# Optimization experiments

Measured on AMD Instinct MI355X. Metric: run time of the kernel, lower is better.

## Reference

```python
import jax, jax.numpy as jnp
import numpy as np
from jax.scipy.ndimage import map_coordinates

H = 256          # detector height (pixels)
W = 256          # detector width (pixels)
PX = 1.6875      # pixel size (mm); W*PX = 432mm
PIERCE = 216.0   # piercing point offset (mm) -> centered detector
SAD = 742.5      # source-to-isocenter distance (mm)
DAD = 517.15     # detector-to-isocenter distance (mm)


def _rotmat(angles):
    # ZYX intrinsic Euler rotation from (alpha, beta, gamma)
    a, b, g = angles[0], angles[1], angles[2]
    ca, sa = jnp.cos(a), jnp.sin(a)
    cb, sb = jnp.cos(b), jnp.sin(b)
    cg, sg = jnp.cos(g), jnp.sin(g)
    Rz = jnp.array([[ca, -sa, 0.], [sa, ca, 0.], [0., 0., 1.]])
    Ry = jnp.array([[cb, 0., sb], [0., 1., 0.], [-sb, 0., cb]])
    Rx = jnp.array([[1., 0., 0.], [0., cg, -sg], [0., sg, cg]])
    return Rz @ Ry @ Rx


def setup_inputs() -> dict:
    key = jax.random.key(0)
    k1, k2 = jax.random.split(key)
    volume = jax.random.uniform(k1, (256, 256, 256), dtype=jnp.float32)  # CT attenuation
    batch = jax.random.normal(k2, (2, 6), dtype=jnp.float32) * 0.1       # [B, (rot3, trans3)]
    return {"volume": volume, "batch": batch, "n_samples": 256}


def reference(volume, batch, n_samples):
    B = batch.shape[0]
    center = jnp.asarray(volume.shape, dtype=volume.dtype) / 2.0  # volume center (mm, unit spacing)

    rots = batch[:, 0:3]
    trans = batch[:, 3:6]
    R = jax.vmap(_rotmat)(rots)                              # [B,3,3]
    iso = center[None, :] + trans                            # [B,3]

    z = jnp.array([0., 0., 1.], dtype=volume.dtype)
    source = iso + SAD * jnp.einsum('bij,j->bi', R, z)       # [B,3]
    det_c = iso - DAD * jnp.einsum('bij,j->bi', R, z)        # [B,3]
    u_ax = R[:, :, 0]                                        # detector u axis [B,3]
    v_ax = R[:, :, 1]                                        # detector v axis [B,3]

    us = (jnp.arange(W, dtype=volume.dtype) * PX - PIERCE)   # [W]
    vs = (jnp.arange(H, dtype=volume.dtype) * PX - PIERCE)   # [H]
    # target pixel positions on detector plane: [B,H,W,3]
    target = (det_c[:, None, None, :]
              + us[None, None, :, None] * u_ax[:, None, None, :]
              + vs[None, :, None, None] * v_ax[:, None, None, :])

    ray = target - source[:, None, None, :]                  # [B,H,W,3]
    length = jnp.linalg.norm(ray, axis=-1)                   # [B,H,W]

    t = jnp.linspace(0.0, 1.0, n_samples, dtype=volume.dtype)  # [S]
    # sample points along each ray: [B,S,H,W,3] (voxel coords, unit spacing)
    pts = source[:, None, None, None, :] + t[None, :, None, None, None] * ray[:, None, :, :, :]

    def sample_one(p):  # p: [S,H,W,3]
        return map_coordinates(volume, [p[..., 0], p[..., 1], p[..., 2]], order=1, mode='constant', cval=0.0)

    samples = jax.vmap(sample_one)(pts)                      # [B,S,H,W]
    img = samples.sum(axis=1) * (length / n_samples)         # line integral [B,H,W]

    img = img.reshape(B, -1)                                 # [B, H*W]
    mn = img.min(axis=1, keepdims=True)
    mx = img.max(axis=1, keepdims=True)
    img = (img - mn) / (mx - mn)
    img = 1.0 - img                                          # bone_dark=True
    return img.reshape(B, H, W)
```

## Files before the change

kernel.cpp:

```cpp
#include <hip/hip_runtime.h>
#include <hip/hip_fp16.h>


static __device__ __constant__ float kPX     = 1.6875f;
static __device__ __constant__ float kPIERCE = 216.0f;
static __device__ __constant__ float kSAD    = 742.5f;
static __device__ __constant__ float kDAD    = 517.15f;

#define VOL_BYTES   (256u * 256u * 256u * 4u)
#define PAIR_R      258u
#define PAIR_ELEMS  (256u * 256u * PAIR_R)
#define PAIR_BYTES  (PAIR_ELEMS * 4u)

typedef __fp16 half2_raw __attribute__((ext_vector_type(2)));

__global__ void drr_init_mm(unsigned* mm) {
    int i = threadIdx.x;
    if (i < 4) mm[i] = (i & 1) ? 0u : 0x7F800000u;
}

__global__ __launch_bounds__(256) void drr_pack(const float* __restrict__ vol,
                                                __half2* __restrict__ vhp,
                                                float* __restrict__ raw) {
    const int bid = blockIdx.x;
    if (threadIdx.x < 32)
        raw[(bid << 5) + threadIdx.x] = 0.0f;

    __shared__ float tile[65][65];
    const int y    = bid >> 4;
    const int t4   = bid & 15;
    const int x0   = (t4 & 3) << 6;
    const int z0   = (t4 >> 2) << 6;

    const int rr = threadIdx.x >> 4;
    const int cc = threadIdx.x & 15;
    #pragma unroll
    for (int base = 0; base < 80; base += 16) {
        const int r = base + rr;
        if (r < 65) {
            const int x = x0 - 1 + r;
            float4 f = make_float4(0.0f, 0.0f, 0.0f, 0.0f);
            if (x >= 0)
                f = *(const float4*)&vol[(x << 16) | (y << 8) | (z0 + (cc << 2))];
            tile[r][(cc << 2) + 0] = f.x;
            tile[r][(cc << 2) + 1] = f.y;
            tile[r][(cc << 2) + 2] = f.z;
            tile[r][(cc << 2) + 3] = f.w;
        }
    }
    __syncthreads();

    const int lane = threadIdx.x & 63;
    const int row4 = threadIdx.x >> 6;
    for (int r = row4; r < 64; r += 4) {
        const int z = z0 + r;
        const unsigned base = (unsigned)((z << 8) | y) * PAIR_R;
        vhp[base + x0 + lane] =
            __halves2half2(__float2half(tile[lane][r]), __float2half(tile[lane + 1][r]));
    }
    if ((t4 & 3) == 3) {
        for (int r = row4; r < 64; r += 4) {
            const int z = z0 + r;
            const unsigned base = (unsigned)((z << 8) | y) * PAIR_R;
            if (lane == 0) {
                vhp[base + 256] = __halves2half2(__float2half(tile[64][r]), __float2half(0.0f));
                vhp[base + 257] = __halves2half2(__float2half(0.0f), __float2half(0.0f));
            }
        }
    }
}

__device__ __forceinline__ void slab(float s, float r, float lo, float hi,
                                     float& tlo, float& thi) {
    if (fabsf(r) > 1e-8f) {
        const float inv = 1.0f / r;
        const float ta  = (lo - s) * inv;
        const float tb  = (hi - s) * inv;
        tlo = fmaxf(tlo, fminf(ta, tb));
        thi = fminf(thi, fmaxf(ta, tb));
    } else if (s < lo || s > hi) {
        tlo = 2.0f; thi = -1.0f;
    }
}

struct RayCfg {
    float rx, ry, rz, length;
    int k_lo, k_hi;
    int s_lo, s_hi;
};

__device__ __forceinline__ void cfg_windows(float sx, float sy, float sz, RayCfg& c) {
    float tlo = 0.0f, thi = 1.0f;
    slab(sx, c.rx, -1.02f, 256.02f, tlo, thi);
    slab(sy, c.ry, -1.02f, 256.02f, tlo, thi);
    slab(sz, c.rz, -1.02f, 256.02f, tlo, thi);
    c.k_lo = 0; c.k_hi = -1;
    if (thi >= tlo) {
        c.k_lo = max(0,   (int)ceilf(tlo * 255.0f - 1e-3f));
        c.k_hi = min(255, (int)floorf(thi * 255.0f + 1e-3f));
    }
    float slo = 0.0f, shi = 1.0f;
    slab(sx, c.rx, 0.01f, 254.99f, slo, shi);
    slab(sy, c.ry, 0.01f, 254.99f, slo, shi);
    slab(sz, c.rz, 0.01f, 254.99f, slo, shi);
    c.s_lo = 1; c.s_hi = -1;
    if (shi >= slo) {
        c.s_lo = (int)ceilf(slo * 255.0f + 1e-3f);
        c.s_hi = (int)floorf(shi * 255.0f - 1e-3f);
    }
}

__device__ __forceinline__ void ray_setup2(const float* __restrict__ batch,
                                           int b, int u, int v0,
                                           float& sx, float& sy, float& sz,
                                           RayCfg& A, RayCfg& B) {
    const float a  = batch[b * 6 + 0];
    const float be = batch[b * 6 + 1];
    const float g  = batch[b * 6 + 2];
    const float tx = batch[b * 6 + 3];
    const float ty = batch[b * 6 + 4];
    const float tz = batch[b * 6 + 5];

    float sa, ca, sb, cb, sg, cg;
    sincosf(a, &sa, &ca);
    sincosf(be, &sb, &cb);
    sincosf(g, &sg, &cg);

    const float R00 = ca * cb;
    const float R01 = ca * sb * sg - sa * cg;
    const float R02 = sa * sg + ca * sb * cg;
    const float R10 = sa * cb;
    const float R11 = ca * cg + sa * sb * sg;
    const float R12 = sa * sb * cg - ca * sg;
    const float R20 = -sb;
    const float R21 = cb * sg;
    const float R22 = cb * cg;

    sx = 128.0f + tx + kSAD * R02;
    sy = 128.0f + ty + kSAD * R12;
    sz = 128.0f + tz + kSAD * R22;

    const float uu = u * kPX - kPIERCE;
    const float vv = v0 * kPX - kPIERCE;
    A.rx = uu * R00 + vv * R01 - (kSAD + kDAD) * R02;
    A.ry = uu * R10 + vv * R11 - (kSAD + kDAD) * R12;
    A.rz = uu * R20 + vv * R21 - (kSAD + kDAD) * R22;
    B.rx = A.rx + kPX * R01;
    B.ry = A.ry + kPX * R11;
    B.rz = A.rz + kPX * R21;
    A.length = sqrtf(A.rx * A.rx + A.ry * A.ry + A.rz * A.rz);
    B.length = sqrtf(B.rx * B.rx + B.ry * B.ry + B.rz * B.rz);
    cfg_windows(sx, sy, sz, A);
    cfg_windows(sx, sy, sz, B);
}

__device__ __forceinline__ float xdot(__half2 q, half2_raw w) {
    return __builtin_amdgcn_fdot2(__builtin_bit_cast(half2_raw, q), w, 0.0f, false);
}

__device__ __forceinline__ float tri_fast(const __half2* __restrict__ vhp,
                                          float sx, float sy, float sz,
                                          const RayCfg& c, float t) {
    const float px = fmaf(t, c.rx, sx);
    const float py = fmaf(t, c.ry, sy);
    const float pz = fmaf(t, c.rz, sz);
    const float fx = floorf(px), fy = floorf(py), fz = floorf(pz);
    const int ix = (int)fx, iy = (int)fy, iz = (int)fz;
    const float wx = px - fx, wy = py - fy, wz = pz - fz;

    const unsigned base = (unsigned)iz * 66048u + (unsigned)iy * 258u + (unsigned)(ix + 1);
    const __half2 q00 = vhp[base];
    const __half2 q01 = vhp[base + 66048u];
    const __half2 q10 = vhp[base + 258u];
    const __half2 q11 = vhp[base + 66306u];

    const half2_raw wxh = __builtin_amdgcn_cvt_pkrtz(1.0f - wx, wx);
    const float a00 = xdot(q00, wxh);
    const float a01 = xdot(q01, wxh);
    const float a10 = xdot(q10, wxh);
    const float a11 = xdot(q11, wxh);

    const float wy0 = 1.0f - wy, wz0 = 1.0f - wz;
    return (a00 * wz0 + a01 * wz) * wy0 + (a10 * wz0 + a11 * wz) * wy;
}

__device__ __forceinline__ float tri_slow(const __half2* __restrict__ vhp,
                                          float sx, float sy, float sz,
                                          const RayCfg& c, float t) {
    const float px = fmaf(t, c.rx, sx);
    const float py = fmaf(t, c.ry, sy);
    const float pz = fmaf(t, c.rz, sz);
    const float fx = floorf(px), fy = floorf(py), fz = floorf(pz);
    const int ix = (int)fx, iy = (int)fy, iz = (int)fz;
    const float wx = px - fx, wy = py - fy, wz = pz - fz;

    const float mx0 = ((unsigned)ix       < 256u) ? 1.0f : 0.0f;
    const float mx1 = ((unsigned)(ix + 1) < 256u) ? 1.0f : 0.0f;
    const float my0 = ((unsigned)iy       < 256u) ? 1.0f : 0.0f;
    const float my1 = ((unsigned)(iy + 1) < 256u) ? 1.0f : 0.0f;
    const float mz0 = ((unsigned)iz       < 256u) ? 1.0f : 0.0f;
    const float mz1 = ((unsigned)(iz + 1) < 256u) ? 1.0f : 0.0f;

    const int i  = min(max(ix + 1, 0), 257);
    const int y0 = min(max(iy,     0), 255);
    const int y1 = min(max(iy + 1, 0), 255);
    const int z0 = min(max(iz,     0), 255);
    const int z1 = min(max(iz + 1, 0), 255);

    const unsigned zt0 = (unsigned)z0 * 66048u;
    const unsigned zt1 = (unsigned)z1 * 66048u;
    const unsigned yt0 = (unsigned)y0 * 258u;
    const unsigned yt1 = (unsigned)y1 * 258u;

    const __half2 q00 = vhp[zt0 + yt0 + i];
    const __half2 q01 = vhp[zt1 + yt0 + i];
    const __half2 q10 = vhp[zt0 + yt1 + i];
    const __half2 q11 = vhp[zt1 + yt1 + i];

    const half2_raw wxh = __builtin_amdgcn_cvt_pkrtz((1.0f - wx) * mx0, wx * mx1);
    const float a00 = xdot(q00, wxh);
    const float a01 = xdot(q01, wxh);
    const float a10 = xdot(q10, wxh);
    const float a11 = xdot(q11, wxh);

    const float wy0 = (1.0f - wy) * my0, wy1 = wy * my1;
    const float wz0 = (1.0f - wz) * mz0, wz1 = wz * mz1;
    return (a00 * wz0 + a01 * wz1) * wy0 + (a10 * wz0 + a11 * wz1) * wy1;
}

__global__ __launch_bounds__(256, 8) void drr_main_pk3(const __half2* __restrict__ vhp,
                                                       const float* __restrict__ batch,
                                                       float* __restrict__ raw) {
    const int tid  = threadIdx.x;
    const int lane = tid & 63;
    const int seg  = tid >> 6;

    const int kq   = blockIdx.x & 3;
    const int tile = blockIdx.x >> 2;
    const int b    = tile >> 9;
    const int ti   = tile & 511;
    const int u    = ((ti & 15) << 4) + (lane & 15);
    const int v0   = ((ti >> 4) << 3) + ((lane >> 4) << 1);

    float sx, sy, sz;
    RayCfg A, B;
    ray_setup2(batch, b, u, v0, sx, sy, sz, A, B);

    const int klo = min(A.k_lo, B.k_lo);
    const int khi = max(A.k_hi, B.k_hi);
    const int slo = max(A.s_lo, B.s_lo);
    const int shi = min(A.s_hi, B.s_hi);

    const float tstep = 1.0f / 255.0f;
    float sA = 0.0f, sB = 0.0f;
    for (int k = klo + (kq << 2) + seg; k <= khi; k += 16) {
        const float t = (float)k * tstep;
        if (k >= slo && k <= shi) {
            sA += tri_fast(vhp, sx, sy, sz, A, t);
            sB += tri_fast(vhp, sx, sy, sz, B, t);
        } else {
            sA += tri_slow(vhp, sx, sy, sz, A, t);
            sB += tri_slow(vhp, sx, sy, sz, B, t);
        }
    }

    __shared__ float pA[4][64], pB[4][64];
    pA[seg][lane] = sA;
    pB[seg][lane] = sB;
    __syncthreads();

    if (tid < 64) {
        const float tA = pA[0][lane] + pA[1][lane] + pA[2][lane] + pA[3][lane];
        const float tB = pB[0][lane] + pB[1][lane] + pB[2][lane] + pB[3][lane];
        if (tA != 0.0f)
            atomicAdd(&raw[(b << 16) + (v0 << 8) + u],       tA * (A.length * (1.0f / 256.0f)));
        if (tB != 0.0f)
            atomicAdd(&raw[(b << 16) + ((v0 + 1) << 8) + u], tB * (B.length * (1.0f / 256.0f)));
    }
}

__global__ __launch_bounds__(256) void drr_minmax(const float* __restrict__ raw,
                                                  float* __restrict__ part) {
    __shared__ float smn[4], smx[4];
    const int gid = blockIdx.x * 256 + threadIdx.x;
    const float x = raw[gid];
    float mn = x, mx = x;
    #pragma unroll
    for (int off = 32; off >= 1; off >>= 1) {
        mn = fminf(mn, __shfl_xor(mn, off));
        mx = fmaxf(mx, __shfl_xor(mx, off));
    }
    if ((threadIdx.x & 63) == 0) {
        smn[threadIdx.x >> 6] = mn;
        smx[threadIdx.x >> 6] = mx;
    }
    __syncthreads();
    if (threadIdx.x == 0) {
        part[2 * blockIdx.x + 0] = fminf(fminf(smn[0], smn[1]), fminf(smn[2], smn[3]));
        part[2 * blockIdx.x + 1] = fmaxf(fmaxf(smx[0], smx[1]), fmaxf(smx[2], smx[3]));
    }
}

__global__ __launch_bounds__(256) void drr_norm(float* __restrict__ img,
                                                const float* __restrict__ part) {
    __shared__ float smn[4], smx[4], fmn, fmx;
    const int b = blockIdx.x >> 8;
    const int pi = (b << 8) + threadIdx.x;
    float mn = part[2 * pi + 0];
    float mx = part[2 * pi + 1];
    #pragma unroll
    for (int off = 32; off >= 1; off >>= 1) {
        mn = fminf(mn, __shfl_xor(mn, off));
        mx = fmaxf(mx, __shfl_xor(mx, off));
    }
    if ((threadIdx.x & 63) == 0) {
        smn[threadIdx.x >> 6] = mn;
        smx[threadIdx.x >> 6] = mx;
    }
    __syncthreads();
    if (threadIdx.x == 0) {
        fmn = fminf(fminf(smn[0], smn[1]), fminf(smn[2], smn[3]));
        fmx = fmaxf(fmaxf(smx[0], smx[1]), fmaxf(smx[2], smx[3]));
    }
    __syncthreads();

    const int gid = blockIdx.x * 256 + threadIdx.x;
    const float inv = 1.0f / (fmx - fmn);
    img[gid] = 1.0f - (img[gid] - fmn) * inv;
}

__global__ __launch_bounds__(256) void drr_transpose(const float* __restrict__ vol,
                                                     float* __restrict__ volt) {
    __shared__ float tile[64][65];
    const int bid  = blockIdx.x;
    const int y    = bid >> 4;
    const int t4   = bid & 15;
    const int x0   = (t4 & 3) << 6;
    const int z0   = (t4 >> 2) << 6;
    const int lane = threadIdx.x & 63;
    const int row4 = threadIdx.x >> 6;

    #pragma unroll
    for (int i = 0; i < 16; ++i) {
        const int xr = (i << 2) + row4;
        tile[xr][lane] = vol[((x0 + xr) << 16) | (y << 8) | (z0 + lane)];
    }
    __syncthreads();
    #pragma unroll
    for (int i = 0; i < 16; ++i) {
        const int zr = (i << 2) + row4;
        volt[((z0 + zr) << 16) | (y << 8) | (x0 + lane)] = tile[lane][zr];
    }
}

__device__ __forceinline__ float tri_sample_f32(const float* __restrict__ vol,
                                                float sx, float sy, float sz,
                                                const RayCfg& c, float t) {
    const float px = fmaf(t, c.rx, sx);
    const float py = fmaf(t, c.ry, sy);
    const float pz = fmaf(t, c.rz, sz);
    const float fx = floorf(px), fy = floorf(py), fz = floorf(pz);
    const int ix = (int)fx, iy = (int)fy, iz = (int)fz;
    const float wx = px - fx, wy = py - fy, wz = pz - fz;
    const float mx0 = ((unsigned)ix       < 256u) ? 1.0f : 0.0f;
    const float mx1 = ((unsigned)(ix + 1) < 256u) ? 1.0f : 0.0f;
    const float my0 = ((unsigned)iy       < 256u) ? 1.0f : 0.0f;
    const float my1 = ((unsigned)(iy + 1) < 256u) ? 1.0f : 0.0f;
    const float mz0 = ((unsigned)iz       < 256u) ? 1.0f : 0.0f;
    const float mz1 = ((unsigned)(iz + 1) < 256u) ? 1.0f : 0.0f;
    const unsigned X0 = (unsigned)ix & 255u, X1 = (unsigned)(ix + 1) & 255u;
    const unsigned Y0 = ((unsigned)iy & 255u) << 8, Y1 = ((unsigned)(iy + 1) & 255u) << 8;
    const unsigned Z0 = ((unsigned)iz & 255u) << 16, Z1 = ((unsigned)(iz + 1) & 255u) << 16;
    const float v000 = vol[Z0 | Y0 | X0];
    const float v001 = vol[Z1 | Y0 | X0];
    const float v010 = vol[Z0 | Y1 | X0];
    const float v011 = vol[Z1 | Y1 | X0];
    const float v100 = vol[Z0 | Y0 | X1];
    const float v101 = vol[Z1 | Y0 | X1];
    const float v110 = vol[Z0 | Y1 | X1];
    const float v111 = vol[Z1 | Y1 | X1];
    const float wx0 = (1.0f - wx) * mx0, wx1 = wx * mx1;
    const float wy0 = (1.0f - wy) * my0, wy1 = wy * my1;
    const float wz0 = (1.0f - wz) * mz0, wz1 = wz * mz1;
    const float c00 = v000 * wz0 + v001 * wz1;
    const float c01 = v010 * wz0 + v011 * wz1;
    const float c10 = v100 * wz0 + v101 * wz1;
    const float c11 = v110 * wz0 + v111 * wz1;
    return (c00 * wy0 + c01 * wy1) * wx0 + (c10 * wy0 + c11 * wy1) * wx1;
}

__global__ __launch_bounds__(256, 4) void drr_main_f32(const float* __restrict__ volt,
                                                       const float* __restrict__ batch,
                                                       float* __restrict__ raw,
                                                       unsigned* __restrict__ mm) {
    const int tid  = threadIdx.x;
    const int lane = tid & 63;
    const int seg  = tid >> 6;
    const int tile = blockIdx.x;
    const int b    = tile >> 10;
    const int ti   = tile & 1023;
    const int u    = ((ti & 15) << 4) + (lane & 15);
    const int v    = ((ti >> 4) << 2) + (lane >> 4);

    float sx, sy, sz;
    RayCfg A, B;
    ray_setup2(batch, b, u, v, sx, sy, sz, A, B);

    const float tstep = 1.0f / 255.0f;
    float sum = 0.0f;
    for (int k = A.k_lo + seg; k <= A.k_hi; k += 4)
        sum += tri_sample_f32(volt, sx, sy, sz, A, (float)k * tstep);

    __shared__ float part[4][64];
    part[seg][lane] = sum;
    __syncthreads();

    if (tid < 64) {
        const float s = part[0][lane] + part[1][lane] + part[2][lane] + part[3][lane];
        const float rawv = s * (A.length * (1.0f / 256.0f));
        raw[(b << 16) + (v << 8) + u] = rawv;
        float mn = rawv, mx = rawv;
        #pragma unroll
        for (int off = 32; off >= 1; off >>= 1) {
            mn = fminf(mn, __shfl_xor(mn, off));
            mx = fmaxf(mx, __shfl_xor(mx, off));
        }
        if (lane == 0) {
            atomicMin(&mm[2 * b + 0], __float_as_uint(mn));
            atomicMax(&mm[2 * b + 1], __float_as_uint(mx));
        }
    }
}

__global__ __launch_bounds__(256) void drr_norm_mm(float* __restrict__ img,
                                                   const unsigned* __restrict__ mm) {
    const int gid = blockIdx.x * 256 + threadIdx.x;
    const int b   = gid >> 16;
    const float mn  = __uint_as_float(mm[2 * b + 0]);
    const float mx  = __uint_as_float(mm[2 * b + 1]);
    const float inv = 1.0f / (mx - mn);
    img[gid] = 1.0f - (img[gid] - mn) * inv;
}

extern "C" void kernel_launch(void* const* d_in, const int* in_sizes, int n_in,
                              void* d_out, int out_size, void* d_ws, size_t ws_size,
                              hipStream_t stream) {
    const float* vol   = (const float*)d_in[0];
    const float* batch = (const float*)d_in[1];
    float* out         = (float*)d_out;

    if (ws_size >= (size_t)PAIR_BYTES + 4096) {
        __half2* vhp  = (__half2*)d_ws;
        float*   part = (float*)((char*)d_ws + PAIR_BYTES);
        drr_pack<<<4096, 256, 0, stream>>>(vol, vhp, out);
        drr_main_pk3<<<4096, 256, 0, stream>>>(vhp, batch, out);
        drr_minmax<<<512, 256, 0, stream>>>(out, part);
        drr_norm<<<512, 256, 0, stream>>>(out, part);
    } else {
        float*    volt = (float*)d_ws;
        unsigned* mm   = (unsigned*)((char*)d_ws + VOL_BYTES);
        drr_init_mm<<<1, 64, 0, stream>>>(mm);
        drr_transpose<<<4096, 256, 0, stream>>>(vol, volt);
        drr_main_f32<<<2048, 256, 0, stream>>>(volt, batch, out, mm);
        drr_norm_mm<<<512, 256, 0, stream>>>(out, mm);
    }
}
```

Measured before the change: 80.12 us.

## Pack volume as fp16 quads covering x and y neighbors for two-load trilinear

Adds a new packing kernel that stores, for each voxel, the x-pair at rows y and y+1 as four fp16 values in one 8-byte uint2, with padded borders. Each trilinear sample then needs two 8-byte loads (z and z+1) instead of four 4-byte loads. The aim is fewer memory transactions per sample in the gather-bound ray-march. In exchange the packed volume is about twice as large, so the pack kernel writes more and the sampling loop's working set grows. The new path is only taken when the workspace is big enough.

Result: slower. 106.4 us (+32.8%).

```diff
diff --git a/kernel.cpp b/kernel.cpp
--- a/kernel.cpp
+++ b/kernel.cpp
@@ -11,12 +11,259 @@
 #define PAIR_R      258u
 #define PAIR_ELEMS  (256u * 256u * PAIR_R)
 #define PAIR_BYTES  (PAIR_ELEMS * 4u)
+#define QJ          258u
+#define QZ          66564u
+#define QUAD_ELEMS  (256u * QJ * QJ)
+#define QUAD_BYTES  ((size_t)QUAD_ELEMS * 8u)
 
 typedef __fp16 half2_raw __attribute__((ext_vector_type(2)));
+
+__device__ __forceinline__ unsigned pack_u(float lo, float hi) {
+    return __builtin_bit_cast(unsigned,
+        __halves2half2(__float2half(lo), __float2half(hi)));
+}
 
 __global__ void drr_init_mm(unsigned* mm) {
     int i = threadIdx.x;
     if (i < 4) mm[i] = (i & 1) ? 0u : 0x7F800000u;
+}
+
+__global__ __launch_bounds__(256) void drr_pack_q(const float* __restrict__ vol,
+                                                  uint2* __restrict__ vq,
+                                                  float* __restrict__ raw) {
+    const int bid = blockIdx.x;
+    if (bid < 4096 && threadIdx.x < 32)
+        raw[(bid << 5) + threadIdx.x] = 0.0f;
+
+    const int j  = bid / 20;
+    const int t  = bid % 20;
+    const int i0 = (t % 5) << 6;
+    const int z0 = (t / 5) << 6;
+
+    __shared__ float tile[2][65][65];
+
+    const int rr = threadIdx.x >> 4;
+    const int cc = threadIdx.x & 15;
+    for (int r = rr; r < 130; r += 16) {
+        const int ysel = (r >= 65) ? 1 : 0;
+        const int xrow = r - ysel * 65;
+        const int x = i0 - 1 + xrow;
+        const int y = j - 1 + ysel;
+        float4 f = make_float4(0.0f, 0.0f, 0.0f, 0.0f);
+        if ((unsigned)x < 256u && (unsigned)y < 256u)
+            f = *(const float4*)&vol[(x << 16) | (y << 8) | (z0 + (cc << 2))];
+        tile[ysel][xrow][(cc << 2) + 0] = f.x;
+        tile[ysel][xrow][(cc << 2) + 1] = f.y;
+        tile[ysel][xrow][(cc << 2) + 2] = f.z;
+        tile[ysel][xrow][(cc << 2) + 3] = f.w;
+    }
+    __syncthreads();
+
+    const int li = threadIdx.x & 63;
+    const int zz = threadIdx.x >> 6;
+    const int i  = i0 + li;
+    if (i < 258) {
+        for (int z = zz; z < 64; z += 4) {
+            const unsigned lo = pack_u(tile[0][li][z], tile[0][li + 1][z]);
+            const unsigned hi = pack_u(tile[1][li][z], tile[1][li + 1][z]);
+            vq[(size_t)(z0 + z) * QZ + (unsigned)j * QJ + i] = make_uint2(lo, hi);
+        }
+    }
+}
+
+__device__ __forceinline__ void slab(float s, float r, float lo, float hi,
+                                     float& tlo, float& thi) {
+    if (fabsf(r) > 1e-8f) {
+        const float inv = 1.0f / r;
+        const float ta  = (lo - s) * inv;
+        const float tb  = (hi - s) * inv;
+        tlo = fmaxf(tlo, fminf(ta, tb));
+        thi = fminf(thi, fmaxf(ta, tb));
+    } else if (s < lo || s > hi) {
+        tlo = 2.0f; thi = -1.0f;
+    }
+}
+
+struct RayCfg {
+    float rx, ry, rz, length;
+    int k_lo, k_hi;
+    int s_lo, s_hi;
+};
+
+__device__ __forceinline__ void cfg_windows(float sx, float sy, float sz, RayCfg& c) {
+    float tlo = 0.0f, thi = 1.0f;
+    slab(sx, c.rx, -1.02f, 256.02f, tlo, thi);
+    slab(sy, c.ry, -1.02f, 256.02f, tlo, thi);
+    slab(sz, c.rz, -1.02f, 256.02f, tlo, thi);
+    c.k_lo = 0; c.k_hi = -1;
+    if (thi >= tlo) {
+        c.k_lo = max(0,   (int)ceilf(tlo * 255.0f - 1e-3f));
+        c.k_hi = min(255, (int)floorf(thi * 255.0f + 1e-3f));
+    }
+    float slo = 0.0f, shi = 1.0f;
+    slab(sx, c.rx, 0.01f, 254.99f, slo, shi);
+    slab(sy, c.ry, 0.01f, 254.99f, slo, shi);
+    slab(sz, c.rz, 0.01f, 254.99f, slo, shi);
+    c.s_lo = 1; c.s_hi = -1;
+    if (shi >= slo) {
+        c.s_lo = (int)ceilf(slo * 255.0f + 1e-3f);
+        c.s_hi = (int)floorf(shi * 255.0f - 1e-3f);
+    }
+}
+
+__device__ __forceinline__ void ray_setup2(const float* __restrict__ batch,
+                                           int b, int u, int v0,
+                                           float& sx, float& sy, float& sz,
+                                           RayCfg& A, RayCfg& B) {
+    const float a  = batch[b * 6 + 0];
+    const float be = batch[b * 6 + 1];
+    const float g  = batch[b * 6 + 2];
+    const float tx = batch[b * 6 + 3];
+    const float ty = batch[b * 6 + 4];
+    const float tz = batch[b * 6 + 5];
+
+    float sa, ca, sb, cb, sg, cg;
+    sincosf(a, &sa, &ca);
+    sincosf(be, &sb, &cb);
+    sincosf(g, &sg, &cg);
+
+    const float R00 = ca * cb;
+    const float R01 = ca * sb * sg - sa * cg;
+    const float R02 = sa * sg + ca * sb * cg;
+    const float R10 = sa * cb;
+    const float R11 = ca * cg + sa * sb * sg;
+    const float R12 = sa * sb * cg - ca * sg;
+    const float R20 = -sb;
+    const float R21 = cb * sg;
+    const float R22 = cb * cg;
+
+    sx = 128.0f + tx + kSAD * R02;
+    sy = 128.0f + ty + kSAD * R12;
+    sz = 128.0f + tz + kSAD * R22;
+
+    const float uu = u * kPX - kPIERCE;
+    const float vv = v0 * kPX - kPIERCE;
+    A.rx = uu * R00 + vv * R01 - (kSAD + kDAD) * R02;
+    A.ry = uu * R10 + vv * R11 - (kSAD + kDAD) * R12;
+    A.rz = uu * R20 + vv * R21 - (kSAD + kDAD) * R22;
+    B.rx = A.rx + kPX * R01;
+    B.ry = A.ry + kPX * R11;
+    B.rz = A.rz + kPX * R21;
+    A.length = sqrtf(A.rx * A.rx + A.ry * A.ry + A.rz * A.rz);
+    B.length = sqrtf(B.rx * B.rx + B.ry * B.ry + B.rz * B.rz);
+    cfg_windows(sx, sy, sz, A);
+    cfg_windows(sx, sy, sz, B);
+}
+
+__device__ __forceinline__ float xdot(unsigned q, half2_raw w) {
+    return __builtin_amdgcn_fdot2(__builtin_bit_cast(half2_raw, q), w, 0.0f, false);
+}
+
+__device__ __forceinline__ float triq_fast(const uint2* __restrict__ vq,
+                                           float sx, float sy, float sz,
+                                           const RayCfg& c, float t) {
+    const float px = fmaf(t, c.rx, sx);
+    const float py = fmaf(t, c.ry, sy);
+    const float pz = fmaf(t, c.rz, sz);
+    const float fx = floorf(px), fy = floorf(py), fz = floorf(pz);
+    const int ix = (int)fx, iy = (int)fy, iz = (int)fz;
+    const float wx = px - fx, wy = py - fy, wz = pz - fz;
+
+    const size_t base = (size_t)iz * QZ + (unsigned)(iy + 1) * QJ + (unsigned)(ix + 1);
+    const uint2 qa = vq[base];
+    const uint2 qb = vq[base + QZ];
+
+    const half2_raw wxh = __builtin_amdgcn_cvt_pkrtz(1.0f - wx, wx);
+    const float a0 = xdot(qa.x, wxh), a1 = xdot(qa.y, wxh);
+    const float b0 = xdot(qb.x, wxh), b1 = xdot(qb.y, wxh);
+
+    const float wy0 = 1.0f - wy, wz0 = 1.0f - wz;
+    return (a0 * wy0 + a1 * wy) * wz0 + (b0 * wy0 + b1 * wy) * wz;
+}
+
+__device__ __forceinline__ float triq_slow(const uint2* __restrict__ vq,
+                                           float sx, float sy, float sz,
+                                           const RayCfg& c, float t) {
+    const float px = fmaf(t, c.rx, sx);
+    const float py = fmaf(t, c.ry, sy);
+    const float pz = fmaf(t, c.rz, sz);
+    const float fx = floorf(px), fy = floorf(py), fz = floorf(pz);
+    const int ix = (int)fx, iy = (int)fy, iz = (int)fz;
+    const float wx = px - fx, wy = py - fy, wz = pz - fz;
+
+    const float mx0 = ((unsigned)ix       < 256u) ? 1.0f : 0.0f;
+    const float mx1 = ((unsigned)(ix + 1) < 256u) ? 1.0f : 0.0f;
+    const float my0 = ((unsigned)iy       < 256u) ? 1.0f : 0.0f;
+    const float my1 = ((unsigned)(iy + 1) < 256u) ? 1.0f : 0.0f;
+    const float mz0 = ((unsigned)iz       < 256u) ? 1.0f : 0.0f;
+    const float mz1 = ((unsigned)(iz + 1) < 256u) ? 1.0f : 0.0f;
+
+    const int i  = min(max(ix + 1, 0), 257);
+    const int jj = min(max(iy + 1, 0), 257);
+    const int z0 = min(max(iz,     0), 255);
+    const int z1 = min(max(iz + 1, 0), 255);
+
+    const uint2 qa = vq[(size_t)z0 * QZ + (unsigned)jj * QJ + i];
+    const uint2 qb = vq[(size_t)z1 * QZ + (unsigned)jj * QJ + i];
+
+    const half2_raw wxh = __builtin_amdgcn_cvt_pkrtz((1.0f - wx) * mx0, wx * mx1);
+    const float a0 = xdot(qa.x, wxh), a1 = xdot(qa.y, wxh);
+    const float b0 = xdot(qb.x, wxh), b1 = xdot(qb.y, wxh);
+
+    const float wy0 = (1.0f - wy) * my0, wy1 = wy * my1;
+    const float wz0 = (1.0f - wz) * mz0, wz1 = wz * mz1;
+    return (a0 * wy0 + a1 * wy1) * wz0 + (b0 * wy0 + b1 * wy1) * wz1;
+}
+
+__global__ __launch_bounds__(256, 8) void drr_main_q(const uint2* __restrict__ vq,
+                                                     const float* __restrict__ batch,
+                                                     float* __restrict__ raw) {
+    const int tid  = threadIdx.x;
+    const int lane = tid & 63;
+    const int seg  = tid >> 6;
+
+    const int kq   = blockIdx.x & 3;
+    const int tile = blockIdx.x >> 2;
+    const int b    = tile >> 9;
+    const int ti   = tile & 511;
+    const int u    = ((ti & 15) << 4) + (lane & 15);
+    const int v0   = ((ti >> 4) << 3) + ((lane >> 4) << 1);
+
+    float sx, sy, sz;
+    RayCfg A, B;
+    ray_setup2(batch, b, u, v0, sx, sy, sz, A, B);
+
+    const int klo = min(A.k_lo, B.k_lo);
+    const int khi = max(A.k_hi, B.k_hi);
+    const int slo = max(A.s_lo, B.s_lo);
+    const int shi = min(A.s_hi, B.s_hi);
+
+    const float tstep = 1.0f / 255.0f;
+    float sA = 0.0f, sB = 0.0f;
+    for (int k = klo + (kq << 2) + seg; k <= khi; k += 16) {
+        const float t = (float)k * tstep;
+        if (k >= slo && k <= shi) {
+            sA += triq_fast(vq, sx, sy, sz, A, t);
+            sB += triq_fast(vq, sx, sy, sz, B, t);
+        } else {
+            sA += triq_slow(vq, sx, sy, sz, A, t);
+            sB += triq_slow(vq, sx, sy, sz, B, t);
+        }
+    }
+
+    __shared__ float pA[4][64], pB[4][64];
+    pA[seg][lane] = sA;
+    pB[seg][lane] = sB;
+    __syncthreads();
+
+    if (tid < 64) {
+        const float tA = pA[0][lane] + pA[1][lane] + pA[2][lane] + pA[3][lane];
+        const float tB = pB[0][lane] + pB[1][lane] + pB[2][lane] + pB[3][lane];
+        if (tA != 0.0f)
+            atomicAdd(&raw[(b << 16) + (v0 << 8) + u],       tA * (A.length * (1.0f / 256.0f)));
+        if (tB != 0.0f)
+            atomicAdd(&raw[(b << 16) + ((v0 + 1) << 8) + u], tB * (B.length * (1.0f / 256.0f)));
+    }
 }
 
 __global__ __launch_bounds__(256) void drr_pack(const float* __restrict__ vol,
@@ -70,91 +317,7 @@
     }
 }
 
-__device__ __forceinline__ void slab(float s, float r, float lo, float hi,
-                                     float& tlo, float& thi) {
-    if (fabsf(r) > 1e-8f) {
-        const float inv = 1.0f / r;
-        const float ta  = (lo - s) * inv;
-        const float tb  = (hi - s) * inv;
-        tlo = fmaxf(tlo, fminf(ta, tb));
-        thi = fminf(thi, fmaxf(ta, tb));
-    } else if (s < lo || s > hi) {
-        tlo = 2.0f; thi = -1.0f;
-    }
-}
-
-struct RayCfg {
-    float rx, ry, rz, length;
-    int k_lo, k_hi;
-    int s_lo, s_hi;
-};
-
-__device__ __forceinline__ void cfg_windows(float sx, float sy, float sz, RayCfg& c) {
-    float tlo = 0.0f, thi = 1.0f;
-    slab(sx, c.rx, -1.02f, 256.02f, tlo, thi);
-    slab(sy, c.ry, -1.02f, 256.02f, tlo, thi);
-    slab(sz, c.rz, -1.02f, 256.02f, tlo, thi);
-    c.k_lo = 0; c.k_hi = -1;
-    if (thi >= tlo) {
-        c.k_lo = max(0,   (int)ceilf(tlo * 255.0f - 1e-3f));
-        c.k_hi = min(255, (int)floorf(thi * 255.0f + 1e-3f));
-    }
-    float slo = 0.0f, shi = 1.0f;
-    slab(sx, c.rx, 0.01f, 254.99f, slo, shi);
-    slab(sy, c.ry, 0.01f, 254.99f, slo, shi);
-    slab(sz, c.rz, 0.01f, 254.99f, slo, shi);
-    c.s_lo = 1; c.s_hi = -1;
-    if (shi >= slo) {
-        c.s_lo = (int)ceilf(slo * 255.0f + 1e-3f);
-        c.s_hi = (int)floorf(shi * 255.0f - 1e-3f);
-    }
-}
-
-__device__ __forceinline__ void ray_setup2(const float* __restrict__ batch,
-                                           int b, int u, int v0,
-                                           float& sx, float& sy, float& sz,
-                                           RayCfg& A, RayCfg& B) {
-    const float a  = batch[b * 6 + 0];
-    const float be = batch[b * 6 + 1];
-    const float g  = batch[b * 6 + 2];
-    const float tx = batch[b * 6 + 3];
-    const float ty = batch[b * 6 + 4];
-    const float tz = batch[b * 6 + 5];
-
-    float sa, ca, sb, cb, sg, cg;
-    sincosf(a, &sa, &ca);
-    sincosf(be, &sb, &cb);
-    sincosf(g, &sg, &cg);
-
-    const float R00 = ca * cb;
-    const float R01 = ca * sb * sg - sa * cg;
-    const float R02 = sa * sg + ca * sb * cg;
-    const float R10 = sa * cb;
-    const float R11 = ca * cg + sa * sb * sg;
-    const float R12 = sa * sb * cg - ca * sg;
-    const float R20 = -sb;
-    const float R21 = cb * sg;
-    const float R22 = cb * cg;
-
-    sx = 128.0f + tx + kSAD * R02;
-    sy = 128.0f + ty + kSAD * R12;
-    sz = 128.0f + tz + kSAD * R22;
-
-    const float uu = u * kPX - kPIERCE;
-    const float vv = v0 * kPX - kPIERCE;
-    A.rx = uu * R00 + vv * R01 - (kSAD + kDAD) * R02;
-    A.ry = uu * R10 + vv * R11 - (kSAD + kDAD) * R12;
-    A.rz = uu * R20 + vv * R21 - (kSAD + kDAD) * R22;
-    B.rx = A.rx + kPX * R01;
-    B.ry = A.ry + kPX * R11;
-    B.rz = A.rz + kPX * R21;
-    A.length = sqrtf(A.rx * A.rx + A.ry * A.ry + A.rz * A.rz);
-    B.length = sqrtf(B.rx * B.rx + B.ry * B.ry + B.rz * B.rz);
-    cfg_windows(sx, sy, sz, A);
-    cfg_windows(sx, sy, sz, B);
-}
-
-__device__ __forceinline__ float xdot(__half2 q, half2_raw w) {
+__device__ __forceinline__ float xdoth(__half2 q, half2_raw w) {
     return __builtin_amdgcn_fdot2(__builtin_bit_cast(half2_raw, q), w, 0.0f, false);
 }
 
@@ -175,10 +338,10 @@
     const __half2 q11 = vhp[base + 66306u];
 
     const half2_raw wxh = __builtin_amdgcn_cvt_pkrtz(1.0f - wx, wx);
-    const float a00 = xdot(q00, wxh);
-    const float a01 = xdot(q01, wxh);
-    const float a10 = xdot(q10, wxh);
-    const float a11 = xdot(q11, wxh);
+    const float a00 = xdoth(q00, wxh);
+    const float a01 = xdoth(q01, wxh);
+    const float a10 = xdoth(q10, wxh);
+    const float a11 = xdoth(q11, wxh);
 
     const float wy0 = 1.0f - wy, wz0 = 1.0f - wz;
     return (a00 * wz0 + a01 * wz) * wy0 + (a10 * wz0 + a11 * wz) * wy;
@@ -218,10 +381,10 @@
     const __half2 q11 = vhp[zt1 + yt1 + i];
 
     const half2_raw wxh = __builtin_amdgcn_cvt_pkrtz((1.0f - wx) * mx0, wx * mx1);
-    const float a00 = xdot(q00, wxh);
-    const float a01 = xdot(q01, wxh);
-    const float a10 = xdot(q10, wxh);
-    const float a11 = xdot(q11, wxh);
+    const float a00 = xdoth(q00, wxh);
+    const float a01 = xdoth(q01, wxh);
+    const float a10 = xdoth(q10, wxh);
+    const float a11 = xdoth(q11, wxh);
 
     const float wy0 = (1.0f - wy) * my0, wy1 = wy * my1;
     const float wz0 = (1.0f - wz) * mz0, wz1 = wz * mz1;
@@ -449,7 +612,14 @@
     const float* batch = (const float*)d_in[1];
     float* out         = (float*)d_out;
 
-    if (ws_size >= (size_t)PAIR_BYTES + 4096) {
+    if (ws_size >= QUAD_BYTES + 4096) {
+        uint2* vq   = (uint2*)d_ws;
+        float* part = (float*)((char*)d_ws + QUAD_BYTES);
+        drr_pack_q<<<5160, 256, 0, stream>>>(vol, vq, out);
+        drr_main_q<<<4096, 256, 0, stream>>>(vq, batch, out);
+        drr_minmax<<<512, 256, 0, stream>>>(out, part);
+        drr_norm<<<512, 256, 0, stream>>>(out, part);
+    } else if (ws_size >= (size_t)PAIR_BYTES + 4096) {
         __half2* vhp  = (__half2*)d_ws;
         float*   part = (float*)((char*)d_ws + PAIR_BYTES);
         drr_pack<<<4096, 256, 0, stream>>>(vol, vhp, out);
```
